# Kernel tuning notes

Measured on AMD Instinct MI355X. Metric: run time of the kernel, lower is better.

Reference implementation:

```python
import jax, jax.numpy as jnp
import numpy as np

N_NODES = 50000
N_EDGES = 800000
IN_DIM = 128
NUM_HEADS = 8
OUT_DIM = 16


def setup_inputs() -> dict:
    key = jax.random.key(0)
    ks = jax.random.split(key, 12)
    s = 1.0 / np.sqrt(IN_DIM)
    return {
        "h": jax.random.normal(ks[0], (N_NODES, IN_DIM), jnp.float32),
        "e": jax.random.normal(ks[1], (N_EDGES, IN_DIM), jnp.float32),
        "src": jax.random.randint(ks[2], (N_EDGES,), 0, N_NODES, jnp.int32),
        "dst": jax.random.randint(ks[3], (N_EDGES,), 0, N_NODES, jnp.int32),
        "Wq": jax.random.normal(ks[4], (IN_DIM, NUM_HEADS * OUT_DIM), jnp.float32) * s,
        "bq": jax.random.normal(ks[5], (NUM_HEADS * OUT_DIM,), jnp.float32) * s,
        "Wk": jax.random.normal(ks[6], (IN_DIM, NUM_HEADS * OUT_DIM), jnp.float32) * s,
        "bk": jax.random.normal(ks[7], (NUM_HEADS * OUT_DIM,), jnp.float32) * s,
        "We": jax.random.normal(ks[8], (IN_DIM, NUM_HEADS * OUT_DIM), jnp.float32) * s,
        "be": jax.random.normal(ks[9], (NUM_HEADS * OUT_DIM,), jnp.float32) * s,
        "Wv": jax.random.normal(ks[10], (IN_DIM, NUM_HEADS * OUT_DIM), jnp.float32) * s,
        "bv": jax.random.normal(ks[11], (NUM_HEADS * OUT_DIM,), jnp.float32) * s,
    }


def reference(h, e, src, dst, Wq, bq, Wk, bk, We, be, Wv, bv):
    N = h.shape[0]
    H, D = NUM_HEADS, OUT_DIM
    Q = (h @ Wq + bq).reshape(N, H, D)
    K = (h @ Wk + bk).reshape(N, H, D)
    V = (h @ Wv + bv).reshape(N, H, D)
    # Edge projection E is computed in the original forward but unused in the score.
    E_proj = (e @ We + be).reshape(-1, H, D)
    del E_proj
    # edge-wise gather + dot-product score: [E, H]
    score = jnp.einsum("ehd,ehd->eh", K[src], Q[dst]) / np.sqrt(D)
    # graph softmax numerator: exp of clamped score, [E, H, 1]
    s = jnp.exp(jnp.clip(score, -5.0, 5.0))[..., None]
    # scatter-sum weighted V and score sums per destination node
    wV = jax.ops.segment_sum(V[src] * s, dst, num_segments=N)  # [N, H, D]
    z = jax.ops.segment_sum(s, dst, num_segments=N)            # [N, H, 1]
    return wV / (z + 1e-6)
```

## Files before the change

### kernel.cpp

```cpp
#include <hip/hip_runtime.h>

#define NN 50000
#define NE 800000

#define QKV_NPB 16
__global__ __launch_bounds__(64) void qkv_kernel(
    const float* __restrict__ h,
    const float* __restrict__ Wq, const float* __restrict__ bq,
    const float* __restrict__ Wk, const float* __restrict__ bk,
    const float* __restrict__ Wv, const float* __restrict__ bv,
    const int* __restrict__ dst, int* __restrict__ counts,
    int* __restrict__ erank,
    float* __restrict__ Q, float* __restrict__ K, float* __restrict__ V)
{
    __shared__ float hs[QKV_NPB * 128];
    const int lane = threadIdx.x;
    const int n0 = blockIdx.x * QKV_NPB;

    {
        const int e0 = blockIdx.x * 256 + lane;
#pragma unroll
        for (int j = 0; j < 4; ++j) {
            const int e = e0 + j * 64;
            erank[e] = atomicAdd(&counts[dst[e]], 1);
        }
    }

    {
        const float4* hsrc = (const float4*)(h + (size_t)n0 * 128);
#pragma unroll
        for (int t = 0; t < 8; ++t) {
            const int idx = lane + t * 64;
            ((float4*)hs)[idx] = hsrc[idx];
        }
    }
    __syncthreads();

    const int c0 = lane * 2;
    float acc[3][2][QKV_NPB];
#pragma unroll
    for (int m = 0; m < 3; ++m)
#pragma unroll
        for (int c = 0; c < 2; ++c)
#pragma unroll
            for (int n = 0; n < QKV_NPB; ++n) acc[m][c][n] = 0.f;

    for (int kk = 0; kk < 128; kk += 4) {
        float2 w[3][4];
#pragma unroll
        for (int j = 0; j < 4; ++j) {
            w[0][j] = *(const float2*)(Wq + (kk + j) * 128 + c0);
            w[1][j] = *(const float2*)(Wk + (kk + j) * 128 + c0);
            w[2][j] = *(const float2*)(Wv + (kk + j) * 128 + c0);
        }
#pragma unroll
        for (int n = 0; n < QKV_NPB; ++n) {
            const float4 hv = *((const float4*)hs + n * 32 + (kk >> 2));
            const float hx[4] = {hv.x, hv.y, hv.z, hv.w};
#pragma unroll
            for (int m = 0; m < 3; ++m)
#pragma unroll
                for (int j = 0; j < 4; ++j) {
                    acc[m][0][n] = fmaf(hx[j], w[m][j].x, acc[m][0][n]);
                    acc[m][1][n] = fmaf(hx[j], w[m][j].y, acc[m][1][n]);
                }
        }
    }

    const float2 b2[3] = { *(const float2*)(bq + c0),
                           *(const float2*)(bk + c0),
                           *(const float2*)(bv + c0) };
    float* const outp[3] = { Q, K, V };
#pragma unroll
    for (int m = 0; m < 3; ++m)
#pragma unroll
        for (int n = 0; n < QKV_NPB; ++n) {
            float2 o = make_float2(acc[m][0][n] + b2[m].x,
                                   acc[m][1][n] + b2[m].y);
            *(float2*)(outp[m] + (size_t)(n0 + n) * 128 + c0) = o;
        }
}

#define SCAN_T 1024
#define SCAN_CHUNK 49
__global__ __launch_bounds__(SCAN_T) void scan_kernel(
    const int* __restrict__ counts, int* __restrict__ offsets)
{
    __shared__ int part[SCAN_T];
    const int t = threadIdx.x;

    int base = t * SCAN_CHUNK;
    int sum = 0;
    for (int j = 0; j < SCAN_CHUNK; ++j) {
        int idx = base + j;
        if (idx < NN) sum += counts[idx];
    }
    part[t] = sum;
    __syncthreads();

    for (int off = 1; off < SCAN_T; off <<= 1) {
        int v = (t >= off) ? part[t - off] : 0;
        __syncthreads();
        part[t] += v;
        __syncthreads();
    }

    int running = (t == 0) ? 0 : part[t - 1];
    for (int j = 0; j < SCAN_CHUNK; ++j) {
        int idx = base + j;
        if (idx < NN) {
            offsets[idx] = running;
            running += counts[idx];
        }
    }
    if (t == SCAN_T - 1) offsets[NN] = part[SCAN_T - 1];
}

__global__ __launch_bounds__(256) void scatter_kernel(
    const int* __restrict__ src, const int* __restrict__ dst,
    const int* __restrict__ offsets, const int* __restrict__ erank,
    int* __restrict__ src_sorted)
{
    const int e = blockIdx.x * 256 + threadIdx.x;
    if (e < NE) {
        const int d = dst[e];
        src_sorted[offsets[d] + erank[e]] = src[e];
    }
}

__global__ __launch_bounds__(256) void aggregate_kernel(
    const int* __restrict__ offsets, const int* __restrict__ src_sorted,
    const float* __restrict__ Q, const float* __restrict__ K,
    const float* __restrict__ V, float* __restrict__ out)
{
    const int n = (blockIdx.x * 256 + threadIdx.x) >> 6;
    if (n >= NN) return;
    const int lane = threadIdx.x & 63;
    const int hh = lane & 7;
    const int es = lane >> 3;

    const float4* Qv = (const float4*)Q + (size_t)n * 32 + hh * 4;
    const float4 q0 = Qv[0], q1 = Qv[1], q2 = Qv[2], q3 = Qv[3];

    float4 a0 = make_float4(0.f, 0.f, 0.f, 0.f);
    float4 a1 = a0, a2 = a0, a3 = a0;
    float z = 0.f;

    const int beg = offsets[n];
    const int end = offsets[n + 1];

    for (int i = beg + es; i < end; i += 8) {
        const int s = src_sorted[i];
        const float4* Kv = (const float4*)K + (size_t)s * 32 + hh * 4;
        const float4* Vv = (const float4*)V + (size_t)s * 32 + hh * 4;
        const float4 k0 = Kv[0], k1 = Kv[1], k2 = Kv[2], k3 = Kv[3];
        const float4 v0 = Vv[0], v1 = Vv[1], v2 = Vv[2], v3 = Vv[3];

        float sc = k0.x * q0.x + k0.y * q0.y + k0.z * q0.z + k0.w * q0.w
                 + k1.x * q1.x + k1.y * q1.y + k1.z * q1.z + k1.w * q1.w
                 + k2.x * q2.x + k2.y * q2.y + k2.z * q2.z + k2.w * q2.w
                 + k3.x * q3.x + k3.y * q3.y + k3.z * q3.z + k3.w * q3.w;
        sc = fminf(5.f, fmaxf(-5.f, sc * 0.25f));
        const float sw = __expf(sc);
        z += sw;
        a0.x = fmaf(sw, v0.x, a0.x); a0.y = fmaf(sw, v0.y, a0.y);
        a0.z = fmaf(sw, v0.z, a0.z); a0.w = fmaf(sw, v0.w, a0.w);
        a1.x = fmaf(sw, v1.x, a1.x); a1.y = fmaf(sw, v1.y, a1.y);
        a1.z = fmaf(sw, v1.z, a1.z); a1.w = fmaf(sw, v1.w, a1.w);
        a2.x = fmaf(sw, v2.x, a2.x); a2.y = fmaf(sw, v2.y, a2.y);
        a2.z = fmaf(sw, v2.z, a2.z); a2.w = fmaf(sw, v2.w, a2.w);
        a3.x = fmaf(sw, v3.x, a3.x); a3.y = fmaf(sw, v3.y, a3.y);
        a3.z = fmaf(sw, v3.z, a3.z); a3.w = fmaf(sw, v3.w, a3.w);
    }

#pragma unroll
    for (int m = 8; m < 64; m <<= 1) {
        z    += __shfl_xor(z,    m, 64);
        a0.x += __shfl_xor(a0.x, m, 64); a0.y += __shfl_xor(a0.y, m, 64);
        a0.z += __shfl_xor(a0.z, m, 64); a0.w += __shfl_xor(a0.w, m, 64);
        a1.x += __shfl_xor(a1.x, m, 64); a1.y += __shfl_xor(a1.y, m, 64);
        a1.z += __shfl_xor(a1.z, m, 64); a1.w += __shfl_xor(a1.w, m, 64);
        a2.x += __shfl_xor(a2.x, m, 64); a2.y += __shfl_xor(a2.y, m, 64);
        a2.z += __shfl_xor(a2.z, m, 64); a2.w += __shfl_xor(a2.w, m, 64);
        a3.x += __shfl_xor(a3.x, m, 64); a3.y += __shfl_xor(a3.y, m, 64);
        a3.z += __shfl_xor(a3.z, m, 64); a3.w += __shfl_xor(a3.w, m, 64);
    }

    const float inv = 1.0f / (z + 1e-6f);
    if (es < 4) {
        float4 r = (es == 0) ? a0 : (es == 1) ? a1 : (es == 2) ? a2 : a3;
        r.x *= inv; r.y *= inv; r.z *= inv; r.w *= inv;
        ((float4*)out)[(size_t)n * 32 + hh * 4 + es] = r;
    }
}

extern "C" void kernel_launch(void* const* d_in, const int* in_sizes, int n_in,
                              void* d_out, int out_size, void* d_ws, size_t ws_size,
                              hipStream_t stream)
{
    const float* h  = (const float*)d_in[0];
    const int* src = (const int*)d_in[2];
    const int* dst = (const int*)d_in[3];
    const float* Wq = (const float*)d_in[4];
    const float* bq = (const float*)d_in[5];
    const float* Wk = (const float*)d_in[6];
    const float* bk = (const float*)d_in[7];
    const float* Wv = (const float*)d_in[10];
    const float* bv = (const float*)d_in[11];

    float* Q = (float*)d_ws;
    float* K = Q + (size_t)NN * 128;
    float* V = K + (size_t)NN * 128;
    int* counts     = (int*)(V + (size_t)NN * 128);
    int* offsets    = counts + NN;
    int* erank      = offsets + (NN + 1);
    int* src_sorted = erank + NE;

    hipMemsetAsync(counts, 0, NN * sizeof(int), stream);

    qkv_kernel<<<NN / QKV_NPB, 64, 0, stream>>>(h, Wq, bq, Wk, bk, Wv, bv,
                                                dst, counts, erank, Q, K, V);
    scan_kernel<<<1, SCAN_T, 0, stream>>>(counts, offsets);
    scatter_kernel<<<(NE + 255) / 256, 256, 0, stream>>>(src, dst, offsets, erank, src_sorted);
    aggregate_kernel<<<(NN * 64) / 256, 256, 0, stream>>>(offsets, src_sorted, Q, K, V, (float*)d_out);
}
```

Baseline: 786.6 us.

## Parallelize offset scan across blocks and unroll aggregate edge loop by two

Replaces the single-block 1024-thread scan, whose per-thread serial chunks give strided, uncoalesced reads, with a three-kernel multi-block scan: per-block reduce, top-level scan of the block sums, then a per-block downsweep. The aggregate kernel now processes two edges per lane per iteration, so more independent K/V gathers are in flight to hide memory latency. The cost is two extra kernel launches and higher register pressure in the aggregate kernel.

```diff
diff --git a/kernel.cpp b/kernel.cpp
--- a/kernel.cpp
+++ b/kernel.cpp
@@ -81,39 +81,62 @@
         }
 }
 
-#define SCAN_T 1024
-#define SCAN_CHUNK 49
-__global__ __launch_bounds__(SCAN_T) void scan_kernel(
-    const int* __restrict__ counts, int* __restrict__ offsets)
-{
-    __shared__ int part[SCAN_T];
+#define SCAN_NB 196
+
+__global__ __launch_bounds__(256) void scan_part_kernel(
+    const int* __restrict__ counts, int* __restrict__ bsum)
+{
+    __shared__ int sm[256];
     const int t = threadIdx.x;
-
-    int base = t * SCAN_CHUNK;
-    int sum = 0;
-    for (int j = 0; j < SCAN_CHUNK; ++j) {
-        int idx = base + j;
-        if (idx < NN) sum += counts[idx];
-    }
-    part[t] = sum;
-    __syncthreads();
-
-    for (int off = 1; off < SCAN_T; off <<= 1) {
-        int v = (t >= off) ? part[t - off] : 0;
-        __syncthreads();
-        part[t] += v;
-        __syncthreads();
-    }
-
-    int running = (t == 0) ? 0 : part[t - 1];
-    for (int j = 0; j < SCAN_CHUNK; ++j) {
-        int idx = base + j;
-        if (idx < NN) {
-            offsets[idx] = running;
-            running += counts[idx];
-        }
-    }
-    if (t == SCAN_T - 1) offsets[NN] = part[SCAN_T - 1];
+    const int idx = blockIdx.x * 256 + t;
+    sm[t] = (idx < NN) ? counts[idx] : 0;
+    __syncthreads();
+#pragma unroll
+    for (int off = 128; off > 0; off >>= 1) {
+        if (t < off) sm[t] += sm[t + off];
+        __syncthreads();
+    }
+    if (t == 0) bsum[blockIdx.x] = sm[0];
+}
+
+__global__ __launch_bounds__(256) void scan_top_kernel(
+    const int* __restrict__ bsum, int* __restrict__ bbase,
+    int* __restrict__ offsets)
+{
+    __shared__ int sm[256];
+    const int t = threadIdx.x;
+    const int v = (t < SCAN_NB) ? bsum[t] : 0;
+    sm[t] = v;
+    __syncthreads();
+#pragma unroll
+    for (int off = 1; off < 256; off <<= 1) {
+        int u = (t >= off) ? sm[t - off] : 0;
+        __syncthreads();
+        sm[t] += u;
+        __syncthreads();
+    }
+    if (t < SCAN_NB) bbase[t] = sm[t] - v;
+    if (t == SCAN_NB - 1) offsets[NN] = sm[t];
+}
+
+__global__ __launch_bounds__(256) void scan_down_kernel(
+    const int* __restrict__ counts, const int* __restrict__ bbase,
+    int* __restrict__ offsets)
+{
+    __shared__ int sm[256];
+    const int t = threadIdx.x;
+    const int idx = blockIdx.x * 256 + t;
+    const int v = (idx < NN) ? counts[idx] : 0;
+    sm[t] = v;
+    __syncthreads();
+#pragma unroll
+    for (int off = 1; off < 256; off <<= 1) {
+        int u = (t >= off) ? sm[t - off] : 0;
+        __syncthreads();
+        sm[t] += u;
+        __syncthreads();
+    }
+    if (idx < NN) offsets[idx] = bbase[blockIdx.x] + sm[t] - v;
 }
 
 __global__ __launch_bounds__(256) void scatter_kernel(
@@ -149,13 +172,56 @@
     const int beg = offsets[n];
     const int end = offsets[n + 1];
 
-    for (int i = beg + es; i < end; i += 8) {
+    int i = beg + es;
+    for (; i + 8 < end; i += 16) {
+        const int s0 = src_sorted[i];
+        const int s1 = src_sorted[i + 8];
+        const float4* K0 = (const float4*)K + (size_t)s0 * 32 + hh * 4;
+        const float4* V0 = (const float4*)V + (size_t)s0 * 32 + hh * 4;
+        const float4* K1 = (const float4*)K + (size_t)s1 * 32 + hh * 4;
+        const float4* V1 = (const float4*)V + (size_t)s1 * 32 + hh * 4;
+        const float4 ka0 = K0[0], ka1 = K0[1], ka2 = K0[2], ka3 = K0[3];
+        const float4 va0 = V0[0], va1 = V0[1], va2 = V0[2], va3 = V0[3];
+        const float4 kb0 = K1[0], kb1 = K1[1], kb2 = K1[2], kb3 = K1[3];
+        const float4 vb0 = V1[0], vb1 = V1[1], vb2 = V1[2], vb3 = V1[3];
+
+        float sc0 = ka0.x * q0.x + ka0.y * q0.y + ka0.z * q0.z + ka0.w * q0.w
+                  + ka1.x * q1.x + ka1.y * q1.y + ka1.z * q1.z + ka1.w * q1.w
+                  + ka2.x * q2.x + ka2.y * q2.y + ka2.z * q2.z + ka2.w * q2.w
+                  + ka3.x * q3.x + ka3.y * q3.y + ka3.z * q3.z + ka3.w * q3.w;
+        float sc1 = kb0.x * q0.x + kb0.y * q0.y + kb0.z * q0.z + kb0.w * q0.w
+                  + kb1.x * q1.x + kb1.y * q1.y + kb1.z * q1.z + kb1.w * q1.w
+                  + kb2.x * q2.x + kb2.y * q2.y + kb2.z * q2.z + kb2.w * q2.w
+                  + kb3.x * q3.x + kb3.y * q3.y + kb3.z * q3.z + kb3.w * q3.w;
+        sc0 = fminf(5.f, fmaxf(-5.f, sc0 * 0.25f));
+        sc1 = fminf(5.f, fmaxf(-5.f, sc1 * 0.25f));
+        const float sw0 = __expf(sc0);
+        const float sw1 = __expf(sc1);
+        z += sw0;
+        a0.x = fmaf(sw0, va0.x, a0.x); a0.y = fmaf(sw0, va0.y, a0.y);
+        a0.z = fmaf(sw0, va0.z, a0.z); a0.w = fmaf(sw0, va0.w, a0.w);
+        a1.x = fmaf(sw0, va1.x, a1.x); a1.y = fmaf(sw0, va1.y, a1.y);
+        a1.z = fmaf(sw0, va1.z, a1.z); a1.w = fmaf(sw0, va1.w, a1.w);
+        a2.x = fmaf(sw0, va2.x, a2.x); a2.y = fmaf(sw0, va2.y, a2.y);
+        a2.z = fmaf(sw0, va2.z, a2.z); a2.w = fmaf(sw0, va2.w, a2.w);
+        a3.x = fmaf(sw0, va3.x, a3.x); a3.y = fmaf(sw0, va3.y, a3.y);
+        a3.z = fmaf(sw0, va3.z, a3.z); a3.w = fmaf(sw0, va3.w, a3.w);
+        z += sw1;
+        a0.x = fmaf(sw1, vb0.x, a0.x); a0.y = fmaf(sw1, vb0.y, a0.y);
+        a0.z = fmaf(sw1, vb0.z, a0.z); a0.w = fmaf(sw1, vb0.w, a0.w);
+        a1.x = fmaf(sw1, vb1.x, a1.x); a1.y = fmaf(sw1, vb1.y, a1.y);
+        a1.z = fmaf(sw1, vb1.z, a1.z); a1.w = fmaf(sw1, vb1.w, a1.w);
+        a2.x = fmaf(sw1, vb2.x, a2.x); a2.y = fmaf(sw1, vb2.y, a2.y);
+        a2.z = fmaf(sw1, vb2.z, a2.z); a2.w = fmaf(sw1, vb2.w, a2.w);
+        a3.x = fmaf(sw1, vb3.x, a3.x); a3.y = fmaf(sw1, vb3.y, a3.y);
+        a3.z = fmaf(sw1, vb3.z, a3.z); a3.w = fmaf(sw1, vb3.w, a3.w);
+    }
+    if (i < end) {
         const int s = src_sorted[i];
         const float4* Kv = (const float4*)K + (size_t)s * 32 + hh * 4;
         const float4* Vv = (const float4*)V + (size_t)s * 32 + hh * 4;
         const float4 k0 = Kv[0], k1 = Kv[1], k2 = Kv[2], k3 = Kv[3];
         const float4 v0 = Vv[0], v1 = Vv[1], v2 = Vv[2], v3 = Vv[3];
-
         float sc = k0.x * q0.x + k0.y * q0.y + k0.z * q0.z + k0.w * q0.w
                  + k1.x * q1.x + k1.y * q1.y + k1.z * q1.z + k1.w * q1.w
                  + k2.x * q2.x + k2.y * q2.y + k2.z * q2.z + k2.w * q2.w
@@ -215,12 +281,16 @@
     int* offsets    = counts + NN;
     int* erank      = offsets + (NN + 1);
     int* src_sorted = erank + NE;
+    int* bsum       = src_sorted + NE;
+    int* bbase      = bsum + SCAN_NB;
 
     hipMemsetAsync(counts, 0, NN * sizeof(int), stream);
 
     qkv_kernel<<<NN / QKV_NPB, 64, 0, stream>>>(h, Wq, bq, Wk, bk, Wv, bv,
                                                 dst, counts, erank, Q, K, V);
-    scan_kernel<<<1, SCAN_T, 0, stream>>>(counts, offsets);
+    scan_part_kernel<<<SCAN_NB, 256, 0, stream>>>(counts, bsum);
+    scan_top_kernel<<<1, 256, 0, stream>>>(bsum, bbase, offsets);
+    scan_down_kernel<<<SCAN_NB, 256, 0, stream>>>(counts, bbase, offsets);
     scatter_kernel<<<(NE + 255) / 256, 256, 0, stream>>>(src, dst, offsets, erank, src_sorted);
     aggregate_kernel<<<(NN * 64) / 256, 256, 0, stream>>>(offsets, src_sorted, Q, K, V, (float*)d_out);
 }
```

Result: faster. 752.1 us (-4.4%).
